# Optimization experiments

Measured on AMD Instinct MI355X. Metric: run time of the kernel, lower is better.

## Reference

```python
import jax, jax.numpy as jnp
import numpy as np

CLAMP_LO, CLAMP_HI = 1e-4, 1.0 - 1e-4
EPS = 1e-8

def setup_inputs() -> dict:
    key = jax.random.key(0)
    k1, k2 = jax.random.split(key)
    B, T, C = 32, 2048, 512
    x = jax.random.normal(k1, (B, T, C), dtype=jnp.float32)
    # init_alpha = 0.9 -> logit(0.9) = log(9), repeated per channel (plus tiny jitter)
    init = jnp.float32(np.log(0.9 / 0.1))
    logit_alpha = init + 0.01 * jax.random.normal(k2, (C,), dtype=jnp.float32)
    return {"x": x, "logit_alpha": logit_alpha}

def reference(x, logit_alpha):
    B, T, C = x.shape
    dt = x.dtype
    a = jnp.clip(jax.nn.sigmoid(logit_alpha), CLAMP_LO, CLAMP_HI).astype(dt)  # [C]
    t = jnp.arange(T, dtype=dt)[:, None]                                      # [T,1]
    a_pow = a[None, :] ** t                                                   # [T,C]
    divisor = jnp.maximum(a_pow, EPS)                                         # [T,C]
    scale = jnp.concatenate(
        [jnp.ones((1, C), dtype=dt), jnp.broadcast_to((1.0 - a)[None, :], (T - 1, C))],
        axis=0,
    )                                                                         # [T,C]
    w = (a_pow * scale)[None]                                                 # [1,T,C]
    y = jnp.cumsum(x * w, axis=1) / divisor[None]                             # [B,T,C]
    return y
```

## Files before the change

### kernel.cpp

```cpp
#include <hip/hip_runtime.h>
#include <math.h>


#define B_ 32
#define T_ 2048
#define C_ 512
#define TB 64
#define NTB (T_ / TB)

typedef float f32x4 __attribute__((ext_vector_type(4)));

__device__ __forceinline__ float clamp_sig(float z) {
    float a = 1.0f / (1.0f + expf(-z));
    return fminf(fmaxf(a, 1e-4f), 1.0f - 1e-4f);
}

__global__ __launch_bounds__(256, 2)
void ema_partials(const float* __restrict__ x,
                  const float* __restrict__ la,
                  float* __restrict__ ws) {
    const int tid = threadIdx.x;
    const int wv = tid >> 6, ln = tid & 63;
    const int b  = blockIdx.x >> 4;
    const int pr = blockIdx.x & 15;
    const int tb = (pr << 1) | (wv >> 1);
    const int c0 = ((wv & 1) << 8) | (ln << 2);
    const int t0 = tb * TB;

    const float4 z4 = *(const float4*)(la + c0);
    float a[4], oma[4], ap[4];
    const float zz[4] = {z4.x, z4.y, z4.z, z4.w};
    #pragma unroll
    for (int j = 0; j < 4; ++j) {
        a[j]   = clamp_sig(zz[j]);
        oma[j] = 1.0f - a[j];
        ap[j]  = exp2f((float)t0 * log2f(a[j]));
    }

    const float4* __restrict__ xp =
        (const float4*)(x + ((size_t)b * T_ + t0) * C_ + c0);
    float s[4] = {0.f, 0.f, 0.f, 0.f};
    #pragma unroll 8
    for (int i = 0; i < TB; ++i) {
        const float4 xv = xp[(size_t)i * (C_ >> 2)];
        const bool z0 = (t0 + i) == 0;
        float w0 = z0 ? 1.0f : ap[0] * oma[0];
        float w1 = z0 ? 1.0f : ap[1] * oma[1];
        float w2 = z0 ? 1.0f : ap[2] * oma[2];
        float w3 = z0 ? 1.0f : ap[3] * oma[3];
        s[0] = fmaf(xv.x, w0, s[0]);
        s[1] = fmaf(xv.y, w1, s[1]);
        s[2] = fmaf(xv.z, w2, s[2]);
        s[3] = fmaf(xv.w, w3, s[3]);
        #pragma unroll
        for (int j = 0; j < 4; ++j) ap[j] *= a[j];
    }
    *(float4*)(ws + (size_t)(b * NTB + tb) * C_ + c0) =
        make_float4(s[0], s[1], s[2], s[3]);
}

__global__ __launch_bounds__(256, 2)
void ema_apply(const float* __restrict__ x,
               const float* __restrict__ la,
               const float* __restrict__ ws,
               float* __restrict__ y) {
    const int tid = threadIdx.x;
    const int wv = tid >> 6, ln = tid & 63;
    const int b  = blockIdx.x >> 4;
    const int pr = blockIdx.x & 15;
    const int tb = (pr << 1) | (wv >> 1);
    const int c0 = ((wv & 1) << 8) | (ln << 2);
    const int t0 = tb * TB;

    const float4 z4 = *(const float4*)(la + c0);
    float a[4], oma[4], ap[4], inva[4], invap[4];
    const float zz[4] = {z4.x, z4.y, z4.z, z4.w};
    #pragma unroll
    for (int j = 0; j < 4; ++j) {
        a[j]     = clamp_sig(zz[j]);
        oma[j]   = 1.0f - a[j];
        const float l2a = log2f(a[j]);
        ap[j]    = exp2f((float)t0 * l2a);
        invap[j] = exp2f(-(float)t0 * l2a);
        inva[j]  = 1.0f / a[j];
    }

    float S[4] = {0.f, 0.f, 0.f, 0.f};
    for (int q = 0; q < tb; ++q) {
        const float4 p = *(const float4*)(ws + (size_t)(b * NTB + q) * C_ + c0);
        S[0] += p.x; S[1] += p.y; S[2] += p.z; S[3] += p.w;
    }

    const float4* __restrict__ xp =
        (const float4*)(x + ((size_t)b * T_ + t0) * C_ + c0);
    float* __restrict__ yp = y + ((size_t)b * T_ + t0) * C_ + c0;

    #pragma unroll 4
    for (int i = 0; i < TB; ++i) {
        const float4 xv = xp[(size_t)i * (C_ >> 2)];
        const bool z0 = (t0 + i) == 0;
        float w0 = z0 ? 1.0f : ap[0] * oma[0];
        float w1 = z0 ? 1.0f : ap[1] * oma[1];
        float w2 = z0 ? 1.0f : ap[2] * oma[2];
        float w3 = z0 ? 1.0f : ap[3] * oma[3];
        S[0] = fmaf(xv.x, w0, S[0]);
        S[1] = fmaf(xv.y, w1, S[1]);
        S[2] = fmaf(xv.z, w2, S[2]);
        S[3] = fmaf(xv.w, w3, S[3]);
        f32x4 out;
        out.x = S[0] * fminf(invap[0], 1e8f);
        out.y = S[1] * fminf(invap[1], 1e8f);
        out.z = S[2] * fminf(invap[2], 1e8f);
        out.w = S[3] * fminf(invap[3], 1e8f);
        __builtin_nontemporal_store(out, (f32x4*)(yp + (size_t)i * C_));
        #pragma unroll
        for (int j = 0; j < 4; ++j) { ap[j] *= a[j]; invap[j] *= inva[j]; }
    }
}

extern "C" void kernel_launch(void* const* d_in, const int* in_sizes, int n_in,
                              void* d_out, int out_size, void* d_ws, size_t ws_size,
                              hipStream_t stream) {
    const float* x  = (const float*)d_in[0];
    const float* la = (const float*)d_in[1];
    float* y  = (float*)d_out;
    float* ws = (float*)d_ws;

    dim3 grid(B_ * (NTB / 2));
    dim3 block(256);
    hipLaunchKernelGGL(ema_partials, grid, block, 0, stream, x, la, ws);
    hipLaunchKernelGGL(ema_apply,    grid, block, 0, stream, x, la, ws, y);
}
```

Measured before the change: 253.0 us.

## Halve time blocks, add separate scan kernel for block carries

Shrinks the time tile from 64 to 32 steps, which doubles the number of blocks and shortens each thread's serial chain. A new middle kernel turns the per-block partial sums into an exclusive prefix sum, so the apply kernel reads one carry value instead of looping over all earlier blocks. The block layout is changed so each block covers all 512 channels over two time tiles, and the launch bound asks for more resident blocks. The cost is a third kernel launch, another pass over the workspace, and a scan kernel that keeps 64 values in registers per thread.

```diff
diff --git a/kernel.cpp b/kernel.cpp
--- a/kernel.cpp
+++ b/kernel.cpp
@@ -2,11 +2,11 @@
 #include <math.h>
 
 
-#define B_ 32
-#define T_ 2048
-#define C_ 512
-#define TB 64
-#define NTB (T_ / TB)
+#define B_   32
+#define T_   2048
+#define C_   512
+#define TB   32
+#define NTB  (T_ / TB)
 
 typedef float f32x4 __attribute__((ext_vector_type(4)));
 
@@ -15,21 +15,22 @@
     return fminf(fmaxf(a, 1e-4f), 1.0f - 1e-4f);
 }
 
-__global__ __launch_bounds__(256, 2)
+__global__ __launch_bounds__(256, 4)
 void ema_partials(const float* __restrict__ x,
                   const float* __restrict__ la,
                   float* __restrict__ ws) {
     const int tid = threadIdx.x;
-    const int wv = tid >> 6, ln = tid & 63;
-    const int b  = blockIdx.x >> 4;
-    const int pr = blockIdx.x & 15;
-    const int tb = (pr << 1) | (wv >> 1);
-    const int c0 = ((wv & 1) << 8) | (ln << 2);
-    const int t0 = tb * TB;
+    const int ct  = tid & 127;
+    const int cs  = tid >> 7;
+    const int b   = blockIdx.x >> 5;
+    const int pr  = blockIdx.x & 31;
+    const int tb  = (pr << 1) | cs;
+    const int c0  = ct << 2;
+    const int t0  = tb * TB;
 
     const float4 z4 = *(const float4*)(la + c0);
+    const float zz[4] = {z4.x, z4.y, z4.z, z4.w};
     float a[4], oma[4], ap[4];
-    const float zz[4] = {z4.x, z4.y, z4.z, z4.w};
     #pragma unroll
     for (int j = 0; j < 4; ++j) {
         a[j]   = clamp_sig(zz[j]);
@@ -44,14 +45,10 @@
     for (int i = 0; i < TB; ++i) {
         const float4 xv = xp[(size_t)i * (C_ >> 2)];
         const bool z0 = (t0 + i) == 0;
-        float w0 = z0 ? 1.0f : ap[0] * oma[0];
-        float w1 = z0 ? 1.0f : ap[1] * oma[1];
-        float w2 = z0 ? 1.0f : ap[2] * oma[2];
-        float w3 = z0 ? 1.0f : ap[3] * oma[3];
-        s[0] = fmaf(xv.x, w0, s[0]);
-        s[1] = fmaf(xv.y, w1, s[1]);
-        s[2] = fmaf(xv.z, w2, s[2]);
-        s[3] = fmaf(xv.w, w3, s[3]);
+        s[0] = fmaf(xv.x, z0 ? 1.0f : ap[0] * oma[0], s[0]);
+        s[1] = fmaf(xv.y, z0 ? 1.0f : ap[1] * oma[1], s[1]);
+        s[2] = fmaf(xv.z, z0 ? 1.0f : ap[2] * oma[2], s[2]);
+        s[3] = fmaf(xv.w, z0 ? 1.0f : ap[3] * oma[3], s[3]);
         #pragma unroll
         for (int j = 0; j < 4; ++j) ap[j] *= a[j];
     }
@@ -59,22 +56,39 @@
         make_float4(s[0], s[1], s[2], s[3]);
 }
 
-__global__ __launch_bounds__(256, 2)
+__global__ __launch_bounds__(256, 4)
+void ema_scanws(float* __restrict__ ws) {
+    const int g = blockIdx.x * 256 + threadIdx.x;
+    const int b = g >> 9, c = g & (C_ - 1);
+    float* __restrict__ p = ws + (size_t)b * NTB * C_ + c;
+    float v[NTB];
+    #pragma unroll
+    for (int k = 0; k < NTB; ++k) v[k] = p[(size_t)k * C_];
+    float run = 0.0f;
+    #pragma unroll
+    for (int k = 0; k < NTB; ++k) {
+        p[(size_t)k * C_] = run;
+        run += v[k];
+    }
+}
+
+__global__ __launch_bounds__(256, 4)
 void ema_apply(const float* __restrict__ x,
                const float* __restrict__ la,
                const float* __restrict__ ws,
                float* __restrict__ y) {
     const int tid = threadIdx.x;
-    const int wv = tid >> 6, ln = tid & 63;
-    const int b  = blockIdx.x >> 4;
-    const int pr = blockIdx.x & 15;
-    const int tb = (pr << 1) | (wv >> 1);
-    const int c0 = ((wv & 1) << 8) | (ln << 2);
-    const int t0 = tb * TB;
+    const int ct  = tid & 127;
+    const int cs  = tid >> 7;
+    const int b   = blockIdx.x >> 5;
+    const int pr  = blockIdx.x & 31;
+    const int tb  = (pr << 1) | cs;
+    const int c0  = ct << 2;
+    const int t0  = tb * TB;
 
     const float4 z4 = *(const float4*)(la + c0);
+    const float zz[4] = {z4.x, z4.y, z4.z, z4.w};
     float a[4], oma[4], ap[4], inva[4], invap[4];
-    const float zz[4] = {z4.x, z4.y, z4.z, z4.w};
     #pragma unroll
     for (int j = 0; j < 4; ++j) {
         a[j]     = clamp_sig(zz[j]);
@@ -85,11 +99,8 @@
         inva[j]  = 1.0f / a[j];
     }
 
-    float S[4] = {0.f, 0.f, 0.f, 0.f};
-    for (int q = 0; q < tb; ++q) {
-        const float4 p = *(const float4*)(ws + (size_t)(b * NTB + q) * C_ + c0);
-        S[0] += p.x; S[1] += p.y; S[2] += p.z; S[3] += p.w;
-    }
+    const float4 p0 = *(const float4*)(ws + (size_t)(b * NTB + tb) * C_ + c0);
+    float S[4] = {p0.x, p0.y, p0.z, p0.w};
 
     const float4* __restrict__ xp =
         (const float4*)(x + ((size_t)b * T_ + t0) * C_ + c0);
@@ -99,14 +110,10 @@
     for (int i = 0; i < TB; ++i) {
         const float4 xv = xp[(size_t)i * (C_ >> 2)];
         const bool z0 = (t0 + i) == 0;
-        float w0 = z0 ? 1.0f : ap[0] * oma[0];
-        float w1 = z0 ? 1.0f : ap[1] * oma[1];
-        float w2 = z0 ? 1.0f : ap[2] * oma[2];
-        float w3 = z0 ? 1.0f : ap[3] * oma[3];
-        S[0] = fmaf(xv.x, w0, S[0]);
-        S[1] = fmaf(xv.y, w1, S[1]);
-        S[2] = fmaf(xv.z, w2, S[2]);
-        S[3] = fmaf(xv.w, w3, S[3]);
+        S[0] = fmaf(xv.x, z0 ? 1.0f : ap[0] * oma[0], S[0]);
+        S[1] = fmaf(xv.y, z0 ? 1.0f : ap[1] * oma[1], S[1]);
+        S[2] = fmaf(xv.z, z0 ? 1.0f : ap[2] * oma[2], S[2]);
+        S[3] = fmaf(xv.w, z0 ? 1.0f : ap[3] * oma[3], S[3]);
         f32x4 out;
         out.x = S[0] * fminf(invap[0], 1e8f);
         out.y = S[1] * fminf(invap[1], 1e8f);
@@ -126,8 +133,10 @@
     float* y  = (float*)d_out;
     float* ws = (float*)d_ws;
 
-    dim3 grid(B_ * (NTB / 2));
-    dim3 block(256);
-    hipLaunchKernelGGL(ema_partials, grid, block, 0, stream, x, la, ws);
-    hipLaunchKernelGGL(ema_apply,    grid, block, 0, stream, x, la, ws, y);
+    hipLaunchKernelGGL(ema_partials, dim3(B_ * (NTB / 2)), dim3(256), 0, stream,
+                       x, la, ws);
+    hipLaunchKernelGGL(ema_scanws,   dim3(B_ * C_ / 256),  dim3(256), 0, stream,
+                       ws);
+    hipLaunchKernelGGL(ema_apply,    dim3(B_ * (NTB / 2)), dim3(256), 0, stream,
+                       x, la, ws, y);
 }
```

After: 255.6 us. Within noise of the previous version (+1.0%).
